# Kernel tuning notes

Measured on AMD Instinct MI355X. Metric: run time of the kernel, lower is better.

Reference implementation:

```python
import jax, jax.numpy as jnp
import numpy as np

MARGIN = 5.0
VAR_FLOOR = 1e-4
BIG = 1e6


def setup_inputs() -> dict:
    key = jax.random.key(0)
    ks = jax.random.split(key, 8)
    B, D, R = 512, 768, 128
    C_new, C_old = 10, 100
    return {
        "features": jax.random.normal(ks[0], (B, D), jnp.float32),
        "labels": jax.random.randint(ks[1], (B,), 0, C_new),
        "new_class_ids": jnp.arange(C_new),
        "cur_means": jax.random.normal(ks[2], (C_new, D), jnp.float32),
        "cur_bases": jax.random.normal(ks[3], (C_new, D, R), jnp.float32),
        "cur_variances": jax.random.uniform(ks[4], (C_new, R + 1), jnp.float32),
        "calibrated_old_means": jax.random.normal(ks[5], (C_old, D), jnp.float32),
        "calibrated_old_bases": jax.random.normal(ks[6], (C_old, D, R), jnp.float32),
        "calibrated_old_variances": jax.random.uniform(ks[7], (C_old, R + 1), jnp.float32),
    }


def _geometry_distance_matrix(z, means, bases, variances):
    # z: [B,D], means: [C,D], bases: [C,D,R], variances: [C,R+1] -> [B,C]
    diff = z[:, None, :] - means[None, :, :]                    # [B,C,D]
    coeff = jnp.einsum('bcd,cdr->bcr', diff, bases)             # [B,C,R]
    eig = jnp.maximum(variances[:, :-1], VAR_FLOOR)             # [C,R]
    res = jnp.maximum(variances[:, -1], VAR_FLOOR)              # [C]
    parallel = jnp.sum(coeff * coeff / eig[None, :, :], axis=-1)  # [B,C]
    recon = jnp.einsum('bcr,cdr->bcd', coeff, bases)            # [B,C,D]
    residual_term = jnp.sum((diff - recon) ** 2, axis=-1) / res[None, :]
    dist = (parallel + residual_term) / z.shape[1]              # normalize_by_dim
    return jnp.nan_to_num(dist, nan=BIG, posinf=BIG, neginf=BIG)


def reference(features, labels, new_class_ids, cur_means, cur_bases, cur_variances,
              calibrated_old_means, calibrated_old_bases, calibrated_old_variances):
    z = jnp.nan_to_num(features, nan=0.0, posinf=0.0, neginf=0.0)  # [B,D]
    labels = labels.reshape(-1)

    own_all = _geometry_distance_matrix(z, cur_means, cur_bases, cur_variances)  # [B,C_new_total]
    old_all = _geometry_distance_matrix(z, calibrated_old_means, calibrated_old_bases,
                                        calibrated_old_variances)               # [B,C_old]
    old_min = jnp.min(old_all, axis=1)                                           # [B]

    # Per-new-class masks; union of class masks reproduces new_mask implicitly.
    masks = (labels[None, :] == new_class_ids[:, None]).astype(z.dtype)          # [K,B]
    counts = masks.sum(axis=1)                                                   # [K]
    denom = jnp.maximum(counts, 1.0)

    own_k = own_all[:, new_class_ids].T                                          # [K,B]
    hinge = jax.nn.relu(MARGIN + own_k - old_min[None, :])                       # [K,B]

    total_k = (hinge * masks).sum(axis=1) / denom
    own_k_mean = (own_k * masks).sum(axis=1) / denom
    old_k_mean = (old_min[None, :] * masks).sum(axis=1) / denom

    valid = (counts > 0).astype(z.dtype)
    n_valid = jnp.maximum(valid.sum(), 1.0)
    total = (total_k * valid).sum() / n_valid
    own = (own_k_mean * valid).sum() / n_valid
    old = (old_k_mean * valid).sum() / n_valid
    return jnp.stack([total, own, old])  # [total, own, old]
```

## Files before the change

kernel.cpp:

```cpp
#include <hip/hip_runtime.h>
#include <hip/hip_bf16.h>
#include <math.h>
#include <stdint.h>

#define B_N   512
#define D_N   768
#define R_N   128
#define C_NEW 10
#define C_OLD 100
#define C_TOT 110
#define MARGIN_F    5.0f
#define VAR_FLOOR_F 1e-4f
#define BIG_F       1e6f

typedef __bf16 bf16;
typedef __bf16 bf16x4 __attribute__((ext_vector_type(4)));
typedef __bf16 bf16x8 __attribute__((ext_vector_type(8)));
typedef float  f32x4  __attribute__((ext_vector_type(4)));

__device__ __forceinline__ float cleanf(float v) { return isfinite(v) ? v : 0.0f; }

__device__ __forceinline__ void gld16(const bf16* g, bf16* l) {
    __builtin_amdgcn_global_load_lds(
        (const __attribute__((address_space(1))) unsigned int*)g,
        (__attribute__((address_space(3))) unsigned int*)l, 16, 0, 0);
}

__global__ __launch_bounds__(256)
void prep_fused(const float* __restrict__ z,
                const float* __restrict__ cur_bases, const float* __restrict__ old_bases,
                const float* __restrict__ cur_means, const float* __restrict__ old_means,
                bf16* __restrict__ zbf, float* __restrict__ znorm,
                bf16* __restrict__ basesT, float* __restrict__ Gacc,
                float* __restrict__ m_c, float* __restrict__ munorm)
{
    const int tid = threadIdx.x, wave = tid >> 6, lane = tid & 63;

    if (blockIdx.x < 128) {
        const int b = blockIdx.x * 4 + wave;
        const float4* src = (const float4*)(z + (size_t)b * D_N);
        bf16x4* dst = (bf16x4*)(zbf + (size_t)b * D_N);
        float nrm = 0.f;
        #pragma unroll
        for (int i = 0; i < 3; ++i) {
            float4 v = src[lane + i * 64];
            v.x = cleanf(v.x); v.y = cleanf(v.y); v.z = cleanf(v.z); v.w = cleanf(v.w);
            nrm += v.x * v.x + v.y * v.y + v.z * v.z + v.w * v.w;
            bf16x4 w;
            w[0] = (bf16)v.x; w[1] = (bf16)v.y; w[2] = (bf16)v.z; w[3] = (bf16)v.w;
            dst[lane + i * 64] = w;
        }
        #pragma unroll
        for (int off = 32; off >= 1; off >>= 1) nrm += __shfl_xor(nrm, off, 64);
        if (lane == 0) znorm[b] = nrm;
        return;
    }

    const int pb = blockIdx.x - 128;
    const int c = pb / 3, part = pb % 3;
    const float* Bc = (c < C_NEW) ? cur_bases + (size_t)c * D_N * R_N
                                  : old_bases + (size_t)(c - C_NEW) * D_N * R_N;
    const float* mu = (c < C_NEW) ? cur_means + (size_t)c * D_N
                                  : old_means + (size_t)(c - C_NEW) * D_N;

    __shared__ bf16 T[128][136];
    __shared__ float sMu[256];
    __shared__ float sRed[256];

    const int quad = lane >> 4, l15 = lane & 15;
    const int wr = (wave >> 1) * 64, wcn = (wave & 1) * 64;
    const int dbase = part * 256;

    {
        float v = mu[dbase + tid];
        sMu[tid] = v;
        float mn = v * v;
        #pragma unroll
        for (int off = 32; off >= 1; off >>= 1) mn += __shfl_xor(mn, off, 64);
        if (lane == 0) sRed[wave] = mn;
    }
    __syncthreads();
    if (tid == 0) atomicAdd(&munorm[c], sRed[0] + sRed[1] + sRed[2] + sRed[3]);

    float mcAcc = 0.f;
    const int mr = tid & 127, mdh = tid >> 7;

    f32x4 acc[4][4];
    #pragma unroll
    for (int i = 0; i < 4; ++i)
        #pragma unroll
        for (int j = 0; j < 4; ++j) acc[i][j] = (f32x4)0.0f;

    for (int ch = 0; ch < 2; ++ch) {
        const int d0 = dbase + ch * 128;
        __syncthreads();
        #pragma unroll
        for (int m = 0; m < 2; ++m) {
            int u = m * 256 + tid;
            int r4 = (u & 31) * 4;
            int dg = u >> 5;
            float4 v[8];
            #pragma unroll
            for (int j = 0; j < 8; ++j)
                v[j] = *(const float4*)(Bc + (size_t)(d0 + dg * 8 + j) * R_N + r4);
            #pragma unroll
            for (int i = 0; i < 4; ++i) {
                bf16x8 w;
                #pragma unroll
                for (int j = 0; j < 8; ++j) {
                    float f = (i == 0) ? v[j].x : (i == 1) ? v[j].y : (i == 2) ? v[j].z : v[j].w;
                    w[j] = (bf16)f;
                }
                *(bf16x8*)&T[r4 + i][dg * 8] = w;
            }
        }
        __syncthreads();
        {
            int r = tid >> 1, hf = tid & 1;
            const uint4* srcp = (const uint4*)&T[r][hf * 64];
            uint4* dstp = (uint4*)(basesT + (size_t)c * R_N * D_N + (size_t)r * D_N + d0 + hf * 64);
            #pragma unroll
            for (int m2 = 0; m2 < 8; ++m2) dstp[m2] = srcp[m2];
        }
        #pragma unroll 8
        for (int k = 0; k < 64; ++k)
            mcAcc += sMu[ch * 128 + mdh * 64 + k] * (float)T[mr][mdh * 64 + k];
        #pragma unroll
        for (int kk = 0; kk < 128; kk += 32) {
            bf16x8 af[4], bg[4];
            #pragma unroll
            for (int i = 0; i < 4; ++i) af[i] = *(const bf16x8*)&T[wr + 16 * i + l15][kk + quad * 8];
            #pragma unroll
            for (int j = 0; j < 4; ++j) bg[j] = *(const bf16x8*)&T[wcn + 16 * j + l15][kk + quad * 8];
            #pragma unroll
            for (int i = 0; i < 4; ++i)
                #pragma unroll
                for (int j = 0; j < 4; ++j)
                    acc[i][j] = __builtin_amdgcn_mfma_f32_16x16x32_bf16(af[i], bg[j], acc[i][j], 0, 0, 0);
        }
    }
    __syncthreads();
    sRed[tid] = mcAcc;
    __syncthreads();
    if (tid < 128) atomicAdd(&m_c[c * R_N + tid], sRed[tid] + sRed[128 + tid]);

    #pragma unroll
    for (int i = 0; i < 4; ++i)
        #pragma unroll
        for (int j = 0; j < 4; ++j)
            #pragma unroll
            for (int reg = 0; reg < 4; ++reg) {
                int r = wr + 16 * i + quad * 4 + reg;
                int s = wcn + 16 * j + l15;
                atomicAdd(&Gacc[(size_t)c * 16384 + (size_t)r * 128 + s], acc[i][j][reg]);
            }
}

#define PADC 136
#define SM_AB  0
#define SM_C   32768
#define SM_M   67584
#define SM_INV 68096
#define SM_PAR 68608
#define SM_CN  69120
#define SM_Q   69632
#define SM_T2  70144
#define SM_MU  73216
#define SM_SZ  74752

__global__ __launch_bounds__(256, 2)
void main_dist(const bf16* __restrict__ zbf, const bf16* __restrict__ basesT,
               const float* __restrict__ Gacc, const float* __restrict__ m_c,
               const float* __restrict__ cur_vars, const float* __restrict__ old_vars,
               const float* __restrict__ cur_means, const float* __restrict__ old_means,
               const float* __restrict__ znorm, const float* __restrict__ munorm,
               float* __restrict__ gdist)
{
    const int mt = blockIdx.x, c = blockIdx.y;
    const int b0 = mt * 128;
    const float* vars = (c < C_NEW) ? cur_vars + (size_t)c * (R_N + 1)
                                    : old_vars + (size_t)(c - C_NEW) * (R_N + 1);
    const float* mu = (c < C_NEW) ? cur_means + (size_t)c * D_N
                                  : old_means + (size_t)(c - C_NEW) * D_N;
    __shared__ __align__(16) unsigned char smem[SM_SZ];
    bf16*  sA   = (bf16*)(smem + SM_AB);
    bf16*  sB   = (bf16*)(smem + SM_AB + 16384);
    bf16*  sG   = (bf16*)(smem + SM_AB);
    bf16*  sC   = (bf16*)(smem + SM_C);
    float* sM   = (float*)(smem + SM_M);
    float* sInv = (float*)(smem + SM_INV);
    float* sPar = (float*)(smem + SM_PAR);
    float* sCn  = (float*)(smem + SM_CN);
    float* sQ   = (float*)(smem + SM_Q);
    float* sT2  = (float*)(smem + SM_T2);
    bf16*  sMuB = (bf16*)(smem + SM_MU);

    const int tid = threadIdx.x, wave = tid >> 6, lane = tid & 63;
    const int quad = lane >> 4, l15 = lane & 15;
    const int wr = (wave >> 1) * 64, wc = (wave & 1) * 64;

    if (tid < 128) {
        sM[tid]   = m_c[c * R_N + tid];
        sInv[tid] = 1.0f / fmaxf(vars[tid], VAR_FLOOR_F);
        sQ[tid]   = 0.0f;
    }
    for (int i = tid; i < D_N; i += 256) sMuB[i] = (bf16)mu[i];

    f32x4 acc1[4][4];
    #pragma unroll
    for (int i = 0; i < 4; ++i)
        #pragma unroll
        for (int j = 0; j < 4; ++j) acc1[i][j] = (f32x4)0.0f;
    float zd = 0.f;
    const int zrow = tid >> 1, zhalf = tid & 1;

    const bf16* Az = zbf + (size_t)b0 * D_N;
    const bf16* Bb = basesT + (size_t)c * R_N * D_N;
    const int rl = lane >> 3;
    const int cl = lane & 7;

    for (int k0 = 0; k0 < D_N; k0 += 64) {
        __syncthreads();
        #pragma unroll
        for (int j = 0; j < 4; ++j) {
            int r0 = j * 32 + wave * 8;
            gld16(Az + (size_t)(r0 + rl) * D_N + k0 + cl * 8, sA + r0 * 64);
            gld16(Bb + (size_t)(r0 + rl) * D_N + k0 + cl * 8, sB + r0 * 64);
        }
        __syncthreads();
        #pragma unroll
        for (int kk = 0; kk < 64; kk += 32) {
            bf16x8 af[4], bg[4];
            #pragma unroll
            for (int i = 0; i < 4; ++i) af[i] = *(const bf16x8*)(sA + (wr + 16 * i + l15) * 64 + kk + quad * 8);
            #pragma unroll
            for (int j = 0; j < 4; ++j) bg[j] = *(const bf16x8*)(sB + (wc + 16 * j + l15) * 64 + kk + quad * 8);
            #pragma unroll
            for (int i = 0; i < 4; ++i)
                #pragma unroll
                for (int j = 0; j < 4; ++j)
                    acc1[i][j] = __builtin_amdgcn_mfma_f32_16x16x32_bf16(af[i], bg[j], acc1[i][j], 0, 0, 0);
        }
        {
            const bf16* zr = sA + zrow * 64 + zhalf * 32;
            const bf16* mr = sMuB + k0 + zhalf * 32;
            #pragma unroll
            for (int m = 0; m < 4; ++m) {
                bf16x8 a = *(const bf16x8*)(zr + m * 8);
                bf16x8 b = *(const bf16x8*)(mr + m * 8);
                #pragma unroll
                for (int e = 0; e < 8; ++e) zd += (float)a[e] * (float)b[e];
            }
        }
    }
    sT2[512 + tid] = zd;

    #pragma unroll
    for (int j = 0; j < 4; ++j) {
        float mcv = sM[wc + 16 * j + l15];
        #pragma unroll
        for (int i = 0; i < 4; ++i)
            #pragma unroll
            for (int reg = 0; reg < 4; ++reg) {
                float cv = acc1[i][j][reg] - mcv;
                acc1[i][j][reg] = cv;
                int row = wr + 16 * i + quad * 4 + reg;
                int col = wc + 16 * j + l15;
                sC[row * PADC + col] = (bf16)cv;
            }
    }
    __syncthreads();

    {
        int row = tid >> 1, half = tid & 1;
        float par = 0.f, cn = 0.f;
        #pragma unroll
        for (int m = 0; m < 8; ++m) {
            bf16x8 v = *(const bf16x8*)(sC + row * PADC + half * 64 + m * 8);
            #pragma unroll
            for (int e = 0; e < 8; ++e) {
                float f = (float)v[e];
                int col = half * 64 + m * 8 + e;
                cn  += f * f;
                par += f * f * sInv[col];
            }
        }
        sT2[tid] = par;
        sT2[256 + tid] = cn;
    }
    {
        const float* Gc = Gacc + (size_t)c * 16384;
        #pragma unroll
        for (int m = 0; m < 16; ++m) {
            int idx = (m * 256 + tid) * 4;
            float4 v = *(const float4*)(Gc + idx);
            bf16x4 w;
            w[0] = (bf16)v.x; w[1] = (bf16)v.y; w[2] = (bf16)v.z; w[3] = (bf16)v.w;
            *(bf16x4*)(sG + idx) = w;
        }
    }
    __syncthreads();
    if (tid < 128) {
        sPar[tid] = sT2[tid * 2] + sT2[tid * 2 + 1];
        sCn[tid]  = sT2[256 + tid * 2] + sT2[256 + tid * 2 + 1];
    }

    f32x4 acc2[4][4];
    #pragma unroll
    for (int i = 0; i < 4; ++i)
        #pragma unroll
        for (int j = 0; j < 4; ++j) acc2[i][j] = (f32x4)0.0f;
    #pragma unroll
    for (int kc = 0; kc < 128; kc += 32) {
        bf16x8 af[4], bg[4];
        #pragma unroll
        for (int i = 0; i < 4; ++i) af[i] = *(const bf16x8*)(sC + (wr + 16 * i + l15) * PADC + kc + quad * 8);
        #pragma unroll
        for (int j = 0; j < 4; ++j) bg[j] = *(const bf16x8*)(sG + (wc + 16 * j + l15) * 128 + kc + quad * 8);
        #pragma unroll
        for (int i = 0; i < 4; ++i)
            #pragma unroll
            for (int j = 0; j < 4; ++j)
                acc2[i][j] = __builtin_amdgcn_mfma_f32_16x16x32_bf16(af[i], bg[j], acc2[i][j], 0, 0, 0);
    }

    #pragma unroll
    for (int i = 0; i < 4; ++i)
        #pragma unroll
        for (int reg = 0; reg < 4; ++reg) {
            float qp = 0.f;
            #pragma unroll
            for (int j = 0; j < 4; ++j) qp += acc2[i][j][reg] * acc1[i][j][reg];
            qp += __shfl_xor(qp, 1, 64);
            qp += __shfl_xor(qp, 2, 64);
            qp += __shfl_xor(qp, 4, 64);
            qp += __shfl_xor(qp, 8, 64);
            if (l15 == 0) atomicAdd(&sQ[wr + 16 * i + quad * 4 + reg], qp);
        }
    __syncthreads();

    if (tid < 128) {
        int b = b0 + tid;
        float zdot = sT2[512 + tid * 2] + sT2[512 + tid * 2 + 1];
        float nd2 = znorm[b] - 2.0f * zdot + munorm[c];
        float res = fmaxf(vars[R_N], VAR_FLOOR_F);
        float dist = (sPar[tid] + (nd2 - 2.0f * sCn[tid] + sQ[tid]) / res) / (float)D_N;
        if (!isfinite(dist)) dist = BIG_F;
        gdist[(size_t)b * C_TOT + c] = dist;
    }
}

__global__ __launch_bounds__(512)
void finalize(const float* __restrict__ gdist,
              const int* __restrict__ labels,
              const int* __restrict__ ncid,
              float* __restrict__ out)
{
    __shared__ float sAcc[C_NEW * 4];
    const int tid = threadIdx.x;
    if (tid < C_NEW * 4) sAcc[tid] = 0.f;
    __syncthreads();

    const float* row = gdist + (size_t)tid * C_TOT;
    float mn = 3.4e38f;
    #pragma unroll
    for (int cc = C_NEW; cc < C_TOT; ++cc) mn = fminf(mn, row[cc]);
    const int lab = labels[tid];
    #pragma unroll
    for (int k = 0; k < C_NEW; ++k) {
        if (lab == ncid[k]) {
            int col = min(max(ncid[k], 0), C_TOT - 1);
            float ow = row[col];
            atomicAdd(&sAcc[k * 4 + 0], 1.0f);
            atomicAdd(&sAcc[k * 4 + 1], fmaxf(0.0f, MARGIN_F + ow - mn));
            atomicAdd(&sAcc[k * 4 + 2], ow);
            atomicAdd(&sAcc[k * 4 + 3], mn);
        }
    }
    __syncthreads();
    if (tid == 0) {
        float total = 0.f, own = 0.f, old = 0.f, nv = 0.f;
        #pragma unroll
        for (int k = 0; k < C_NEW; ++k) {
            float cnt = sAcc[k * 4 + 0];
            float den = fmaxf(cnt, 1.0f);
            if (cnt > 0.f) {
                nv += 1.f;
                total += sAcc[k * 4 + 1] / den;
                own   += sAcc[k * 4 + 2] / den;
                old   += sAcc[k * 4 + 3] / den;
            }
        }
        float nvd = fmaxf(nv, 1.0f);
        out[0] = total / nvd;
        out[1] = own / nvd;
        out[2] = old / nvd;
    }
}

extern "C" void kernel_launch(void* const* d_in, const int* in_sizes, int n_in,
                              void* d_out, int out_size, void* d_ws, size_t ws_size,
                              hipStream_t stream)
{
    const float* features  = (const float*)d_in[0];
    const int*   labels    = (const int*)d_in[1];
    const int*   ncid      = (const int*)d_in[2];
    const float* cur_means = (const float*)d_in[3];
    const float* cur_bases = (const float*)d_in[4];
    const float* cur_vars  = (const float*)d_in[5];
    const float* old_means = (const float*)d_in[6];
    const float* old_bases = (const float*)d_in[7];
    const float* old_vars  = (const float*)d_in[8];

    unsigned char* ws = (unsigned char*)d_ws;
    float* gdist  = (float*)(ws + 0);
    bf16*  zbf    = (bf16*) (ws + 225280);
    float* znorm  = (float*)(ws + 1011712);
    float* munorm = (float*)(ws + 1013760);
    float* m_c    = (float*)(ws + 1014272);
    float* Gacc   = (float*)(ws + 1070592);
    bf16*  basesT = (bf16*) (ws + 8279552);

    hipMemsetAsync(munorm, 0, 512 + 56320 + 7208960, stream);

    prep_fused<<<dim3(128 + 3 * C_TOT), dim3(256), 0, stream>>>(
        features, cur_bases, old_bases, cur_means, old_means,
        zbf, znorm, basesT, Gacc, m_c, munorm);
    main_dist<<<dim3(4, C_TOT), dim3(256), 0, stream>>>(zbf, basesT, Gacc, m_c,
                                                        cur_vars, old_vars,
                                                        cur_means, old_means,
                                                        znorm, munorm, gdist);
    finalize<<<dim3(1), dim3(512), 0, stream>>>(gdist, labels, ncid, (float*)d_out);
}
```

Measured before the change: 172.5 us.

## Compute z·mu for all classes with an MFMA GEMM in prep kernel

Moves the per-row z·mu dot product out of main_dist's k-loop, where it ran as scalar bf16 FMAs over LDS, into four extra prep_fused blocks. Those blocks compute a 512x110 GEMM of cleaned z against all class means with MFMA and write it to a workspace buffer. main_dist then reads one value per row, drops the mean staging and the scalar loop, and uses slightly less shared memory. In exchange prep_fused gains four long-running blocks that re-read z from fp32, plus an extra global buffer round trip.

```diff
diff --git a/kernel.cpp b/kernel.cpp
--- a/kernel.cpp
+++ b/kernel.cpp
@@ -32,9 +32,11 @@
                 const float* __restrict__ cur_means, const float* __restrict__ old_means,
                 bf16* __restrict__ zbf, float* __restrict__ znorm,
                 bf16* __restrict__ basesT, float* __restrict__ Gacc,
-                float* __restrict__ m_c, float* __restrict__ munorm)
+                float* __restrict__ m_c, float* __restrict__ munorm,
+                float* __restrict__ zdotmu)
 {
     const int tid = threadIdx.x, wave = tid >> 6, lane = tid & 63;
+    __shared__ __align__(16) unsigned char sm[36864];
 
     if (blockIdx.x < 128) {
         const int b = blockIdx.x * 4 + wave;
@@ -56,6 +58,77 @@
         return;
     }
 
+    const int quad = lane >> 4, l15 = lane & 15;
+    const int wr = (wave >> 1) * 64, wcn = (wave & 1) * 64;
+
+    if (blockIdx.x >= 458) {
+        const int zt = blockIdx.x - 458;
+        const int b0 = zt * 128;
+        bf16* sZ = (bf16*)sm;
+        bf16* sU = (bf16*)(sm + 16384);
+
+        f32x4 acc[4][4];
+        #pragma unroll
+        for (int i = 0; i < 4; ++i)
+            #pragma unroll
+            for (int j = 0; j < 4; ++j) acc[i][j] = (f32x4)0.0f;
+
+        for (int k0 = 0; k0 < D_N; k0 += 64) {
+            __syncthreads();
+            #pragma unroll
+            for (int p = 0; p < 8; ++p) {
+                int q = p * 256 + tid;
+                int row = q >> 4, col4 = (q & 15) * 4;
+                float4 v = *(const float4*)(z + (size_t)(b0 + row) * D_N + k0 + col4);
+                bf16x4 w;
+                w[0] = (bf16)cleanf(v.x); w[1] = (bf16)cleanf(v.y);
+                w[2] = (bf16)cleanf(v.z); w[3] = (bf16)cleanf(v.w);
+                *(bf16x4*)(sZ + row * 64 + col4) = w;
+            }
+            #pragma unroll
+            for (int p = 0; p < 8; ++p) {
+                int q = p * 256 + tid;
+                int row = q >> 4, col4 = (q & 15) * 4;
+                bf16x4 w;
+                if (row < C_TOT) {
+                    const float* mp = (row < C_NEW) ? cur_means + (size_t)row * D_N
+                                                    : old_means + (size_t)(row - C_NEW) * D_N;
+                    float4 v = *(const float4*)(mp + k0 + col4);
+                    w[0] = (bf16)v.x; w[1] = (bf16)v.y; w[2] = (bf16)v.z; w[3] = (bf16)v.w;
+                } else {
+                    w[0] = (bf16)0.f; w[1] = (bf16)0.f; w[2] = (bf16)0.f; w[3] = (bf16)0.f;
+                }
+                *(bf16x4*)(sU + row * 64 + col4) = w;
+            }
+            __syncthreads();
+            #pragma unroll
+            for (int kk = 0; kk < 64; kk += 32) {
+                bf16x8 af[4], bg[4];
+                #pragma unroll
+                for (int i = 0; i < 4; ++i) af[i] = *(const bf16x8*)(sZ + (wr + 16 * i + l15) * 64 + kk + quad * 8);
+                #pragma unroll
+                for (int j = 0; j < 4; ++j) bg[j] = *(const bf16x8*)(sU + (wcn + 16 * j + l15) * 64 + kk + quad * 8);
+                #pragma unroll
+                for (int i = 0; i < 4; ++i)
+                    #pragma unroll
+                    for (int j = 0; j < 4; ++j)
+                        acc[i][j] = __builtin_amdgcn_mfma_f32_16x16x32_bf16(af[i], bg[j], acc[i][j], 0, 0, 0);
+            }
+        }
+        #pragma unroll
+        for (int i = 0; i < 4; ++i)
+            #pragma unroll
+            for (int j = 0; j < 4; ++j)
+                #pragma unroll
+                for (int reg = 0; reg < 4; ++reg) {
+                    int row = wr + 16 * i + quad * 4 + reg;
+                    int col = wcn + 16 * j + l15;
+                    if (col < C_TOT)
+                        zdotmu[(size_t)(b0 + row) * C_TOT + col] = acc[i][j][reg];
+                }
+        return;
+    }
+
     const int pb = blockIdx.x - 128;
     const int c = pb / 3, part = pb % 3;
     const float* Bc = (c < C_NEW) ? cur_bases + (size_t)c * D_N * R_N
@@ -63,12 +136,10 @@
     const float* mu = (c < C_NEW) ? cur_means + (size_t)c * D_N
                                   : old_means + (size_t)(c - C_NEW) * D_N;
 
-    __shared__ bf16 T[128][136];
-    __shared__ float sMu[256];
-    __shared__ float sRed[256];
-
-    const int quad = lane >> 4, l15 = lane & 15;
-    const int wr = (wave >> 1) * 64, wcn = (wave & 1) * 64;
+    bf16 (*T)[136] = (bf16(*)[136])sm;
+    float* sMu  = (float*)(sm + 34816);
+    float* sRed = (float*)(sm + 34816 + 1024);
+
     const int dbase = part * 256;
 
     {
@@ -165,23 +236,19 @@
 #define SM_CN  69120
 #define SM_Q   69632
 #define SM_T2  70144
-#define SM_MU  73216
-#define SM_SZ  74752
+#define SM_SZ  72192
 
 __global__ __launch_bounds__(256, 2)
 void main_dist(const bf16* __restrict__ zbf, const bf16* __restrict__ basesT,
                const float* __restrict__ Gacc, const float* __restrict__ m_c,
                const float* __restrict__ cur_vars, const float* __restrict__ old_vars,
-               const float* __restrict__ cur_means, const float* __restrict__ old_means,
                const float* __restrict__ znorm, const float* __restrict__ munorm,
-               float* __restrict__ gdist)
+               const float* __restrict__ zdotmu, float* __restrict__ gdist)
 {
     const int mt = blockIdx.x, c = blockIdx.y;
     const int b0 = mt * 128;
     const float* vars = (c < C_NEW) ? cur_vars + (size_t)c * (R_N + 1)
                                     : old_vars + (size_t)(c - C_NEW) * (R_N + 1);
-    const float* mu = (c < C_NEW) ? cur_means + (size_t)c * D_N
-                                  : old_means + (size_t)(c - C_NEW) * D_N;
     __shared__ __align__(16) unsigned char smem[SM_SZ];
     bf16*  sA   = (bf16*)(smem + SM_AB);
     bf16*  sB   = (bf16*)(smem + SM_AB + 16384);
@@ -193,7 +260,6 @@
     float* sCn  = (float*)(smem + SM_CN);
     float* sQ   = (float*)(smem + SM_Q);
     float* sT2  = (float*)(smem + SM_T2);
-    bf16*  sMuB = (bf16*)(smem + SM_MU);
 
     const int tid = threadIdx.x, wave = tid >> 6, lane = tid & 63;
     const int quad = lane >> 4, l15 = lane & 15;
@@ -204,15 +270,12 @@
         sInv[tid] = 1.0f / fmaxf(vars[tid], VAR_FLOOR_F);
         sQ[tid]   = 0.0f;
     }
-    for (int i = tid; i < D_N; i += 256) sMuB[i] = (bf16)mu[i];
 
     f32x4 acc1[4][4];
     #pragma unroll
     for (int i = 0; i < 4; ++i)
         #pragma unroll
         for (int j = 0; j < 4; ++j) acc1[i][j] = (f32x4)0.0f;
-    float zd = 0.f;
-    const int zrow = tid >> 1, zhalf = tid & 1;
 
     const bf16* Az = zbf + (size_t)b0 * D_N;
     const bf16* Bb = basesT + (size_t)c * R_N * D_N;
@@ -241,19 +304,7 @@
                 for (int j = 0; j < 4; ++j)
                     acc1[i][j] = __builtin_amdgcn_mfma_f32_16x16x32_bf16(af[i], bg[j], acc1[i][j], 0, 0, 0);
         }
-        {
-            const bf16* zr = sA + zrow * 64 + zhalf * 32;
-            const bf16* mr = sMuB + k0 + zhalf * 32;
-            #pragma unroll
-            for (int m = 0; m < 4; ++m) {
-                bf16x8 a = *(const bf16x8*)(zr + m * 8);
-                bf16x8 b = *(const bf16x8*)(mr + m * 8);
-                #pragma unroll
-                for (int e = 0; e < 8; ++e) zd += (float)a[e] * (float)b[e];
-            }
-        }
-    }
-    sT2[512 + tid] = zd;
+    }
 
     #pragma unroll
     for (int j = 0; j < 4; ++j) {
@@ -341,7 +392,7 @@
 
     if (tid < 128) {
         int b = b0 + tid;
-        float zdot = sT2[512 + tid * 2] + sT2[512 + tid * 2 + 1];
+        float zdot = zdotmu[(size_t)b * C_TOT + c];
         float nd2 = znorm[b] - 2.0f * zdot + munorm[c];
         float res = fmaxf(vars[R_N], VAR_FLOOR_F);
         float dist = (sPar[tid] + (nd2 - 2.0f * sCn[tid] + sQ[tid]) / res) / (float)D_N;
@@ -420,15 +471,15 @@
     float* m_c    = (float*)(ws + 1014272);
     float* Gacc   = (float*)(ws + 1070592);
     bf16*  basesT = (bf16*) (ws + 8279552);
+    float* zdotmu = (float*)(ws + 29906432);
 
     hipMemsetAsync(munorm, 0, 512 + 56320 + 7208960, stream);
 
-    prep_fused<<<dim3(128 + 3 * C_TOT), dim3(256), 0, stream>>>(
+    prep_fused<<<dim3(128 + 3 * C_TOT + 4), dim3(256), 0, stream>>>(
         features, cur_bases, old_bases, cur_means, old_means,
-        zbf, znorm, basesT, Gacc, m_c, munorm);
+        zbf, znorm, basesT, Gacc, m_c, munorm, zdotmu);
     main_dist<<<dim3(4, C_TOT), dim3(256), 0, stream>>>(zbf, basesT, Gacc, m_c,
                                                         cur_vars, old_vars,
-                                                        cur_means, old_means,
-                                                        znorm, munorm, gdist);
+                                                        znorm, munorm, zdotmu, gdist);
     finalize<<<dim3(1), dim3(512), 0, stream>>>(gdist, labels, ncid, (float*)d_out);
 }
```

Result: slower. 191.2 us (+10.9%).
